# Kernel optimization log

Measured on AMD Instinct MI355X. Metric: run time of the kernel, lower is better.

## Reference

```python
import jax, jax.numpy as jnp
import numpy as np

EMBED_DIM = 512
N_HEAD = 8
Q_DIM = 64
V_DIM = 64
WINDOW_SIZE = 3


def setup_inputs() -> dict:
    key = jax.random.key(0)
    ks = jax.random.split(key, 9)
    B, N = 2, 2048
    x = jax.random.normal(ks[0], (B, N, EMBED_DIM), dtype=jnp.float32)
    s = 0.02
    # torch nn.Linear weights are [out_features, in_features]; y = x @ W.T + b
    Wq = jax.random.normal(ks[1], (N_HEAD * Q_DIM, EMBED_DIM), dtype=jnp.float32) * s
    bq = jax.random.normal(ks[2], (N_HEAD * Q_DIM,), dtype=jnp.float32) * s
    Wk = jax.random.normal(ks[3], (N_HEAD * Q_DIM, EMBED_DIM), dtype=jnp.float32) * s
    bk = jax.random.normal(ks[4], (N_HEAD * Q_DIM,), dtype=jnp.float32) * s
    Wv = jax.random.normal(ks[5], (N_HEAD * V_DIM, EMBED_DIM), dtype=jnp.float32) * s
    bv = jax.random.normal(ks[6], (N_HEAD * V_DIM,), dtype=jnp.float32) * s
    Wo = jax.random.normal(ks[7], (EMBED_DIM, N_HEAD * V_DIM), dtype=jnp.float32) * s
    bo = jax.random.normal(ks[8], (EMBED_DIM,), dtype=jnp.float32) * s
    return {"x": x, "Wq": Wq, "bq": bq, "Wk": Wk, "bk": bk,
            "Wv": Wv, "bv": bv, "Wo": Wo, "bo": bo}


def _diag_indices(n_seq, di):
    # rows i and cols j = i + di of the di-th diagonal
    if di >= 0:
        ii = np.arange(0, n_seq - di)
    else:
        ii = np.arange(-di, n_seq)
    return ii, ii + di


def reference(x, Wq, bq, Wk, bk, Wv, bv, Wo, bo):
    B, N, E = x.shape
    H, Dq, Dv = N_HEAD, Q_DIM, V_DIM
    Q = (x @ Wq.T + bq).reshape(B, N, H, Dq).transpose(0, 2, 1, 3)  # [B,H,N,Dq]
    K = (x @ Wk.T + bk).reshape(B, N, H, Dq).transpose(0, 2, 1, 3)
    V = (x @ Wv.T + bv).reshape(B, N, H, Dv).transpose(0, 2, 1, 3)  # [B,H,N,Dv]
    half = WINDOW_SIZE // 2
    # Faithful to source: scores scattered into COLUMN index i (the loop
    # counter), not the key position; all other columns remain 0 and still
    # participate in the full softmax over n_seq.
    columns = jnp.zeros((B, H, N, N), dtype=x.dtype)
    for i, di in enumerate(range(-half, half + 1)):
        ii, jj = _diag_indices(N, di)
        c = jnp.einsum('bhid,bhid->bhi', Q[:, :, ii, :], K[:, :, jj, :])
        columns = columns.at[:, :, ii, i].set(c)
    attn = jax.nn.softmax(columns, axis=-1)          # [B,H,N,N]
    out = attn @ V                                    # [B,H,N,Dv]
    out = out.transpose(0, 2, 1, 3).reshape(B, N, H * Dv)
    return out @ Wo.T + bo
```

## Files before the change

### kernel.cpp

```cpp
#include <hip/hip_runtime.h>
#include <hip/hip_bf16.h>

#define EMBED 512
#define NSEQ 2048
#define NROWS 4096

typedef unsigned short u16;
typedef __bf16 bf16x8 __attribute__((ext_vector_type(8)));
typedef float f32x4 __attribute__((ext_vector_type(4)));
typedef unsigned short ushort8 __attribute__((ext_vector_type(8)));

__device__ __forceinline__ u16 f2bf(float f) {
    unsigned u = __float_as_uint(f);
    unsigned r = (u + 0x7FFFu + ((u >> 16) & 1u)) >> 16;
    return (u16)r;
}
__device__ __forceinline__ float bf2f(u16 v) {
    return __uint_as_float((unsigned)v << 16);
}

#define XELEMS    (NROWS * EMBED)
#define WCATELEMS (1536 * EMBED)
#define NCONVB    1408

__global__ __launch_bounds__(256) void prep_kernel(
    const float* __restrict__ x,
    const float* __restrict__ Wq, const float* __restrict__ Wk,
    const float* __restrict__ Wv,
    u16* __restrict__ xb, u16* __restrict__ Wcat)
{
    const long long e0 = (long long)(blockIdx.x * 256 + threadIdx.x) * 8;
    const float* src;
    u16* dst;
    if (e0 < XELEMS) {
        src = x + e0; dst = xb + e0;
    } else {
        const long long j = e0 - XELEMS;
        const int row = (int)(j >> 9);
        const int col = (int)(j & 511);
        const int sel = row >> 9;
        const int r   = row & 511;
        const float* W = (sel == 0) ? Wq : (sel == 1) ? Wk : Wv;
        src = W + (size_t)r * EMBED + col; dst = Wcat + j;
    }
    float4 a = *(const float4*)(src);
    float4 b = *(const float4*)(src + 4);
    union { u16 u[8]; uint4 v; } p;
    p.u[0] = f2bf(a.x); p.u[1] = f2bf(a.y); p.u[2] = f2bf(a.z); p.u[3] = f2bf(a.w);
    p.u[4] = f2bf(b.x); p.u[5] = f2bf(b.y); p.u[6] = f2bf(b.z); p.u[7] = f2bf(b.w);
    *(uint4*)(dst) = p.v;
}

__global__ __launch_bounds__(256) void gemm_qkv_mfma(
    const u16* __restrict__ A, const u16* __restrict__ W,
    const float* __restrict__ bq, const float* __restrict__ bk,
    const float* __restrict__ bvv,
    u16* __restrict__ QKb, float* __restrict__ Vhead,
    float* __restrict__ vpart)
{
    __shared__ __align__(16) u16 As[128 * 64];
    __shared__ __align__(16) u16 Bs[64 * 64];

    const int m0 = (blockIdx.x & 31) * 128;
    const int n0 = (blockIdx.x >> 5) * 64;
    const int sel = n0 >> 9;
    const float* bias = ((sel == 0) ? bq : (sel == 1) ? bk : bvv) + (n0 & 511);

    const int t    = threadIdx.x;
    const int wave = t >> 6, lane = t & 63;
    const int wm   = wave >> 1, wn = wave & 1;
    const int qd   = lane >> 4, lr = lane & 15;

    const int sr8 = lane >> 3;
    const int sg  = (lane & 7) ^ sr8;
    const int soff = sg * 8;

    f32x4 acc[4][2] = {};

    const u16* Ag = A + (size_t)m0 * EMBED;
    const u16* Wg = W + (size_t)n0 * EMBED;

    u16* Adst = As + (size_t)(wave * 8) * 64;
    u16* Bdst = Bs + (size_t)(wave * 8) * 64;
    const u16* Asrc = Ag + (size_t)(wave * 8 + sr8) * EMBED + soff;
    const u16* Bsrc = Wg + (size_t)(wave * 8 + sr8) * EMBED + soff;

    for (int kc = 0; kc < EMBED; kc += 64) {
#pragma unroll
        for (int j = 0; j < 4; ++j)
            __builtin_amdgcn_global_load_lds(
                (const __attribute__((address_space(1))) void*)(Asrc + kc + (size_t)j * 32 * EMBED),
                (__attribute__((address_space(3))) void*)(Adst + j * 32 * 64), 16, 0, 0);
#pragma unroll
        for (int j = 0; j < 2; ++j)
            __builtin_amdgcn_global_load_lds(
                (const __attribute__((address_space(1))) void*)(Bsrc + kc + (size_t)j * 32 * EMBED),
                (__attribute__((address_space(3))) void*)(Bdst + j * 32 * 64), 16, 0, 0);
        __syncthreads();

#pragma unroll
        for (int kk = 0; kk < 2; ++kk) {
            const int gr = ((kk * 4 + qd) ^ (lr & 7)) * 8;
            bf16x8 af[4], bfr[2];
#pragma unroll
            for (int i = 0; i < 4; ++i)
                af[i]  = *(const bf16x8*)&As[(wm * 64 + i * 16 + lr) * 64 + gr];
#pragma unroll
            for (int i = 0; i < 2; ++i)
                bfr[i] = *(const bf16x8*)&Bs[(wn * 32 + i * 16 + lr) * 64 + gr];
#pragma unroll
            for (int mi = 0; mi < 4; ++mi)
#pragma unroll
                for (int ni = 0; ni < 2; ++ni)
                    acc[mi][ni] = __builtin_amdgcn_mfma_f32_16x16x32_bf16(
                        af[mi], bfr[ni], acc[mi][ni], 0, 0, 0);
        }
        __syncthreads();
    }

    if (sel < 2) {
#pragma unroll
        for (int ni = 0; ni < 2; ++ni) {
            const int cl = wn * 32 + ni * 16 + lr;
            const float bb = bias[cl];
#pragma unroll
            for (int mi = 0; mi < 4; ++mi)
#pragma unroll
                for (int e = 0; e < 4; ++e) {
                    const int row = m0 + wm * 64 + mi * 16 + qd * 4 + e;
                    QKb[(size_t)row * 1024 + n0 + cl] = f2bf(acc[mi][ni][e] + bb);
                }
        }
    } else {
        const int batch = m0 >> 11;
        const int mtb   = (m0 >> 7) & 15;
#pragma unroll
        for (int ni = 0; ni < 2; ++ni) {
            const int cl  = wn * 32 + ni * 16 + lr;
            const int col = (n0 - 1024) + cl;
            const float bb = bias[cl];
            float s = 0.f;
#pragma unroll
            for (int mi = 0; mi < 4; ++mi)
#pragma unroll
                for (int e = 0; e < 4; ++e) {
                    const int row = m0 + wm * 64 + mi * 16 + qd * 4 + e;
                    s += acc[mi][ni][e];
                    if ((row & (NSEQ - 1)) < 3)
                        Vhead[(size_t)batch * 1536 + (row & (NSEQ - 1)) * 512 + col]
                            = acc[mi][ni][e] + bb;
                }
            s += __shfl_xor(s, 16);
            s += __shfl_xor(s, 32);
            if (qd == 0)
                vpart[((size_t)batch * 512 + col) * 32 + mtb * 2 + wm] = s;
        }
    }
}

__global__ __launch_bounds__(256) void wsmall_kernel(
    const float* __restrict__ Vhead, const float* __restrict__ vpart,
    const float* __restrict__ bv,
    const float* __restrict__ Wo, float* __restrict__ WT)
{
    __shared__ float Vsm[4][512];
    const int b  = blockIdx.x >> 6;
    const int jb = blockIdx.x & 63;
    const int t  = threadIdx.x;

    for (int idx = t; idx < 512; idx += 256) {
        const float v0 = Vhead[(size_t)b * 1536 + idx];
        const float v1 = Vhead[(size_t)b * 1536 + 512 + idx];
        const float v2 = Vhead[(size_t)b * 1536 + 1024 + idx];
        float sum = 0.f;
        const float* vp = vpart + ((size_t)b * 512 + idx) * 32;
#pragma unroll
        for (int s = 0; s < 32; ++s) sum += vp[s];
        Vsm[0][idx] = v0; Vsm[1][idx] = v1; Vsm[2][idx] = v2;
        Vsm[3][idx] = sum + (float)NSEQ * bv[idx] - (v0 + v1 + v2);
    }
    __syncthreads();

    const int j  = jb * 8 + (t >> 5);
    const int s  = t & 31;
    const int h  = s >> 2, tt = s & 3;
    const float* Wor = Wo + (size_t)j * EMBED + h * 64;
    const float* vr  = &Vsm[tt][h * 64];
    float acc = 0.f;
#pragma unroll
    for (int c = 0; c < 64; ++c) {
        const int cc = (c + 2 * s) & 63;
        acc = fmaf(vr[cc], Wor[cc], acc);
    }
    WT[((size_t)b * 512 + j) * 32 + s] = acc;
}

__global__ __launch_bounds__(256) void attn_out_kernel(
    const u16* __restrict__ QKb, const float* __restrict__ WT,
    const float* __restrict__ bo, float* __restrict__ out)
{
    __shared__ float E[16][32];
    const int r0   = blockIdx.x * 16;
    const int b    = r0 >> 11;
    const int wave = threadIdx.x >> 6, lane = threadIdx.x & 63;
    const int d0   = lane * 8;

#pragma unroll
    for (int i = 0; i < 4; ++i) {
        const int rl = wave * 4 + i;
        const int r  = r0 + rl;
        const int sr = r & (NSEQ - 1);
        const u16* Qr = QKb + (size_t)r * 1024 + d0;
        const u16* Kr = QKb + (size_t)r * 1024 + 512 + d0;

        ushort8 qv = *(const ushort8*)Qr;
        ushort8 kv = *(const ushort8*)Kr;
        float q[8], k[8];
#pragma unroll
        for (int z = 0; z < 8; ++z) { q[z] = bf2f(qv[z]); k[z] = bf2f(kv[z]); }

        float s1 = 0.f;
#pragma unroll
        for (int z = 0; z < 8; ++z) s1 = fmaf(q[z], k[z], s1);

        float s0 = 0.f, s2 = 0.f;
        if (sr > 0) {
            ushort8 pv = *(const ushort8*)(Kr - 1024);
#pragma unroll
            for (int z = 0; z < 8; ++z) s0 = fmaf(q[z], bf2f(pv[z]), s0);
        }
        if (sr < NSEQ - 1) {
            ushort8 nv = *(const ushort8*)(Kr + 1024);
#pragma unroll
            for (int z = 0; z < 8; ++z) s2 = fmaf(q[z], bf2f(nv[z]), s2);
        }
#pragma unroll
        for (int off = 1; off <= 4; off <<= 1) {
            s0 += __shfl_xor(s0, off);
            s1 += __shfl_xor(s1, off);
            s2 += __shfl_xor(s2, off);
        }
        const float m  = fmaxf(fmaxf(s0, s1), fmaxf(s2, 0.f));
        const float e0 = __expf(s0 - m);
        const float e1 = __expf(s1 - m);
        const float e2 = __expf(s2 - m);
        const float eb = __expf(-m);
        const float rd = 1.f / (e0 + e1 + e2 + (float)(NSEQ - 3) * eb);
        const int h = lane >> 3, jj = lane & 7;
        const float coef = (jj == 0) ? e0 : (jj == 1) ? e1 : (jj == 2) ? e2 : eb;
        if (jj < 4) E[rl][h * 4 + jj] = coef * rd;
    }
    __syncthreads();

    const int j0 = threadIdx.x * 2;
    const float* WTb = WT + (size_t)b * 512 * 32;
    float w0[32], w1[32];
#pragma unroll
    for (int s = 0; s < 32; ++s) {
        w0[s] = WTb[(size_t)j0 * 32 + s];
        w1[s] = WTb[(size_t)(j0 + 1) * 32 + s];
    }
    const float b0 = bo[j0], b1 = bo[j0 + 1];
#pragma unroll
    for (int rl = 0; rl < 16; ++rl) {
        float a0 = b0, a1 = b1;
#pragma unroll
        for (int s = 0; s < 32; ++s) {
            const float e = E[rl][s];
            a0 = fmaf(e, w0[s], a0);
            a1 = fmaf(e, w1[s], a1);
        }
        float2 o = make_float2(a0, a1);
        *(float2*)(out + (size_t)(r0 + rl) * EMBED + j0) = o;
    }
}

extern "C" void kernel_launch(void* const* d_in, const int* in_sizes, int n_in,
                              void* d_out, int out_size, void* d_ws, size_t ws_size,
                              hipStream_t stream)
{
    const float* x  = (const float*)d_in[0];
    const float* Wq = (const float*)d_in[1];
    const float* bq = (const float*)d_in[2];
    const float* Wk = (const float*)d_in[3];
    const float* bk = (const float*)d_in[4];
    const float* Wv = (const float*)d_in[5];
    const float* bv = (const float*)d_in[6];
    const float* Wo = (const float*)d_in[7];
    const float* bo = (const float*)d_in[8];
    float* out = (float*)d_out;

    u16*   QKb   = (u16*)d_ws;
    u16*   xb    = QKb + (size_t)NROWS * 1024;
    u16*   Wcat  = xb + XELEMS;
    float* Vhead = (float*)(Wcat + WCATELEMS);
    float* vpart = Vhead + 2 * 3 * 512;
    float* WT    = vpart + 2 * 512 * 32;

    prep_kernel<<<NCONVB, 256, 0, stream>>>(x, Wq, Wk, Wv, xb, Wcat);
    gemm_qkv_mfma<<<768, 256, 0, stream>>>(xb, Wcat, bq, bk, bv, QKb, Vhead, vpart);
    wsmall_kernel<<<128, 256, 0, stream>>>(Vhead, vpart, bv, Wo, WT);
    attn_out_kernel<<<256, 256, 0, stream>>>(QKb, WT, bo, out);
}
```

Measured before the change: 105.7 us.

## Replace V projection GEMM with column-sum trick and fold Wo fold into GEMM kernel

```diff
diff --git a/kernel.cpp b/kernel.cpp
--- a/kernel.cpp
+++ b/kernel.cpp
@@ -20,53 +20,152 @@
 }
 
 #define XELEMS    (NROWS * EMBED)
-#define WCATELEMS (1536 * EMBED)
-#define NCONVB    1408
+#define WQKELEMS  (1024 * EMBED)
 
 __global__ __launch_bounds__(256) void prep_kernel(
     const float* __restrict__ x,
     const float* __restrict__ Wq, const float* __restrict__ Wk,
-    const float* __restrict__ Wv,
-    u16* __restrict__ xb, u16* __restrict__ Wcat)
+    u16* __restrict__ xb, u16* __restrict__ Wcat,
+    float* __restrict__ xcs_part)
 {
-    const long long e0 = (long long)(blockIdx.x * 256 + threadIdx.x) * 8;
-    const float* src;
-    u16* dst;
-    if (e0 < XELEMS) {
-        src = x + e0; dst = xb + e0;
+    __shared__ float cs[4][512];
+    const int bid = blockIdx.x, t = threadIdx.x;
+    if (bid < 256) {
+        const float* src = x + (size_t)bid * 16 * EMBED;
+        u16* dst = xb + (size_t)bid * 16 * EMBED;
+        const int rl = t >> 6;
+        const int co = (t & 63) * 8;
+        float s0=0.f,s1=0.f,s2=0.f,s3=0.f,s4=0.f,s5=0.f,s6=0.f,s7=0.f;
+#pragma unroll
+        for (int i = 0; i < 4; ++i) {
+            const size_t off = (size_t)(i * 4 + rl) * EMBED + co;
+            float4 a = *(const float4*)(src + off);
+            float4 b = *(const float4*)(src + off + 4);
+            union { u16 u[8]; uint4 v; } p;
+            p.u[0]=f2bf(a.x); p.u[1]=f2bf(a.y); p.u[2]=f2bf(a.z); p.u[3]=f2bf(a.w);
+            p.u[4]=f2bf(b.x); p.u[5]=f2bf(b.y); p.u[6]=f2bf(b.z); p.u[7]=f2bf(b.w);
+            *(uint4*)(dst + off) = p.v;
+            s0+=a.x; s1+=a.y; s2+=a.z; s3+=a.w;
+            s4+=b.x; s5+=b.y; s6+=b.z; s7+=b.w;
+        }
+        f32x4 v0 = {s0,s1,s2,s3}, v1 = {s4,s5,s6,s7};
+        *(f32x4*)&cs[rl][co]     = v0;
+        *(f32x4*)&cs[rl][co + 4] = v1;
+        __syncthreads();
+        const int b = bid >> 7, blk = bid & 127;
+#pragma unroll
+        for (int d = t; d < 512; d += 256) {
+            xcs_part[((size_t)b * 512 + d) * 128 + blk] =
+                cs[0][d] + cs[1][d] + cs[2][d] + cs[3][d];
+        }
     } else {
-        const long long j = e0 - XELEMS;
-        const int row = (int)(j >> 9);
-        const int col = (int)(j & 511);
-        const int sel = row >> 9;
-        const int r   = row & 511;
-        const float* W = (sel == 0) ? Wq : (sel == 1) ? Wk : Wv;
-        src = W + (size_t)r * EMBED + col; dst = Wcat + j;
-    }
-    float4 a = *(const float4*)(src);
-    float4 b = *(const float4*)(src + 4);
-    union { u16 u[8]; uint4 v; } p;
-    p.u[0] = f2bf(a.x); p.u[1] = f2bf(a.y); p.u[2] = f2bf(a.z); p.u[3] = f2bf(a.w);
-    p.u[4] = f2bf(b.x); p.u[5] = f2bf(b.y); p.u[6] = f2bf(b.z); p.u[7] = f2bf(b.w);
-    *(uint4*)(dst) = p.v;
-}
-
-__global__ __launch_bounds__(256) void gemm_qkv_mfma(
+        const long long e0 = (long long)(bid - 256) * 2048 + (long long)t * 8;
+        const int row = (int)(e0 >> 9), col = (int)(e0 & 511);
+        const float* src = (row < 512) ? (Wq + (size_t)row * EMBED + col)
+                                       : (Wk + (size_t)(row - 512) * EMBED + col);
+        float4 a = *(const float4*)(src);
+        float4 b = *(const float4*)(src + 4);
+        union { u16 u[8]; uint4 v; } p;
+        p.u[0]=f2bf(a.x); p.u[1]=f2bf(a.y); p.u[2]=f2bf(a.z); p.u[3]=f2bf(a.w);
+        p.u[4]=f2bf(b.x); p.u[5]=f2bf(b.y); p.u[6]=f2bf(b.z); p.u[7]=f2bf(b.w);
+        *(uint4*)(Wcat + e0) = p.v;
+    }
+}
+
+__global__ __launch_bounds__(256) void gemm_qk_mfma(
     const u16* __restrict__ A, const u16* __restrict__ W,
     const float* __restrict__ bq, const float* __restrict__ bk,
-    const float* __restrict__ bvv,
-    u16* __restrict__ QKb, float* __restrict__ Vhead,
-    float* __restrict__ vpart)
+    const float* __restrict__ xcs_part, const float* __restrict__ bv,
+    const float* __restrict__ Wv, const float* __restrict__ Wo,
+    u16* __restrict__ QKb, float* __restrict__ WT)
 {
     __shared__ __align__(16) u16 As[128 * 64];
     __shared__ __align__(16) u16 Bs[64 * 64];
+    const int t = threadIdx.x;
+
+    if (blockIdx.x >= 512) {
+        float* xcs  = (float*)As;
+        float* Vraw = (float*)Bs;
+        float* Vloc = Vraw + 256;
+        const int sid = blockIdx.x - 512;
+        const int b = sid >> 4, h = (sid >> 1) & 7, jhalf = sid & 1;
+
+        {
+            const float* p = xcs_part + ((size_t)b * 512 + 2 * t) * 128;
+            float a0 = 0.f, a1 = 0.f;
+#pragma unroll 4
+            for (int i = 0; i < 128; i += 4) {
+                f32x4 u0 = *(const f32x4*)(p + i);
+                f32x4 u1 = *(const f32x4*)(p + 128 + i);
+                a0 += u0[0] + u0[1] + u0[2] + u0[3];
+                a1 += u1[0] + u1[1] + u1[2] + u1[3];
+            }
+            xcs[2 * t] = a0; xcs[2 * t + 1] = a1;
+        }
+        __syncthreads();
+
+        const int tt = t >> 6, cl = t & 63;
+        const int col = h * 64 + cl;
+        const float* wv = Wv + (size_t)col * EMBED;
+        float r = 0.f;
+        if (tt < 3) {
+            const u16* xr = A + ((size_t)b * NSEQ + tt) * EMBED;
+#pragma unroll 8
+            for (int d = 0; d < EMBED; d += 8) {
+                ushort8 xv = *(const ushort8*)(xr + d);
+                f32x4 w0 = *(const f32x4*)(wv + d);
+                f32x4 w1 = *(const f32x4*)(wv + d + 4);
+                r = fmaf(bf2f(xv[0]), w0[0], r);
+                r = fmaf(bf2f(xv[1]), w0[1], r);
+                r = fmaf(bf2f(xv[2]), w0[2], r);
+                r = fmaf(bf2f(xv[3]), w0[3], r);
+                r = fmaf(bf2f(xv[4]), w1[0], r);
+                r = fmaf(bf2f(xv[5]), w1[1], r);
+                r = fmaf(bf2f(xv[6]), w1[2], r);
+                r = fmaf(bf2f(xv[7]), w1[3], r);
+            }
+        } else {
+#pragma unroll 8
+            for (int d = 0; d < EMBED; d += 4) {
+                f32x4 w = *(const f32x4*)(wv + d);
+                r = fmaf(xcs[d],     w[0], r);
+                r = fmaf(xcs[d + 1], w[1], r);
+                r = fmaf(xcs[d + 2], w[2], r);
+                r = fmaf(xcs[d + 3], w[3], r);
+            }
+        }
+        Vraw[tt * 64 + cl] = r;
+        __syncthreads();
+        const float bvc = bv[col];
+        if (tt < 3) Vloc[tt * 64 + cl] = r + bvc;
+        else        Vloc[192 + cl] = r - (Vraw[cl] + Vraw[64 + cl] + Vraw[128 + cl])
+                                       + 2045.f * bvc;
+        __syncthreads();
+
+        const int j = jhalf * 256 + t;
+        const float* wo = Wo + (size_t)j * EMBED + h * 64;
+        float a0 = 0.f, a1 = 0.f, a2 = 0.f, a3 = 0.f;
+#pragma unroll
+        for (int c = 0; c < 64; c += 4) {
+            f32x4 w = *(const f32x4*)(wo + c);
+#pragma unroll
+            for (int z = 0; z < 4; ++z) {
+                a0 = fmaf(Vloc[c + z],       w[z], a0);
+                a1 = fmaf(Vloc[64 + c + z],  w[z], a1);
+                a2 = fmaf(Vloc[128 + c + z], w[z], a2);
+                a3 = fmaf(Vloc[192 + c + z], w[z], a3);
+            }
+        }
+        float* wt = WT + ((size_t)b * 512 + j) * 32 + h * 4;
+        wt[0] = a0; wt[1] = a1; wt[2] = a2; wt[3] = a3;
+        return;
+    }
 
     const int m0 = (blockIdx.x & 31) * 128;
     const int n0 = (blockIdx.x >> 5) * 64;
     const int sel = n0 >> 9;
-    const float* bias = ((sel == 0) ? bq : (sel == 1) ? bk : bvv) + (n0 & 511);
-
-    const int t    = threadIdx.x;
+    const float* bias = ((sel == 0) ? bq : bk) + (n0 & 511);
+
     const int wave = t >> 6, lane = t & 63;
     const int wm   = wave >> 1, wn = wave & 1;
     const int qd   = lane >> 4, lr = lane & 15;
@@ -118,96 +217,33 @@
         __syncthreads();
     }
 
-    if (sel < 2) {
-#pragma unroll
-        for (int ni = 0; ni < 2; ++ni) {
-            const int cl = wn * 32 + ni * 16 + lr;
-            const float bb = bias[cl];
-#pragma unroll
-            for (int mi = 0; mi < 4; ++mi)
-#pragma unroll
-                for (int e = 0; e < 4; ++e) {
-                    const int row = m0 + wm * 64 + mi * 16 + qd * 4 + e;
-                    QKb[(size_t)row * 1024 + n0 + cl] = f2bf(acc[mi][ni][e] + bb);
-                }
-        }
-    } else {
-        const int batch = m0 >> 11;
-        const int mtb   = (m0 >> 7) & 15;
-#pragma unroll
-        for (int ni = 0; ni < 2; ++ni) {
-            const int cl  = wn * 32 + ni * 16 + lr;
-            const int col = (n0 - 1024) + cl;
-            const float bb = bias[cl];
-            float s = 0.f;
-#pragma unroll
-            for (int mi = 0; mi < 4; ++mi)
-#pragma unroll
-                for (int e = 0; e < 4; ++e) {
-                    const int row = m0 + wm * 64 + mi * 16 + qd * 4 + e;
-                    s += acc[mi][ni][e];
-                    if ((row & (NSEQ - 1)) < 3)
-                        Vhead[(size_t)batch * 1536 + (row & (NSEQ - 1)) * 512 + col]
-                            = acc[mi][ni][e] + bb;
-                }
-            s += __shfl_xor(s, 16);
-            s += __shfl_xor(s, 32);
-            if (qd == 0)
-                vpart[((size_t)batch * 512 + col) * 32 + mtb * 2 + wm] = s;
-        }
-    }
-}
-
-__global__ __launch_bounds__(256) void wsmall_kernel(
-    const float* __restrict__ Vhead, const float* __restrict__ vpart,
-    const float* __restrict__ bv,
-    const float* __restrict__ Wo, float* __restrict__ WT)
-{
-    __shared__ float Vsm[4][512];
-    const int b  = blockIdx.x >> 6;
-    const int jb = blockIdx.x & 63;
-    const int t  = threadIdx.x;
-
-    for (int idx = t; idx < 512; idx += 256) {
-        const float v0 = Vhead[(size_t)b * 1536 + idx];
-        const float v1 = Vhead[(size_t)b * 1536 + 512 + idx];
-        const float v2 = Vhead[(size_t)b * 1536 + 1024 + idx];
-        float sum = 0.f;
-        const float* vp = vpart + ((size_t)b * 512 + idx) * 32;
-#pragma unroll
-        for (int s = 0; s < 32; ++s) sum += vp[s];
-        Vsm[0][idx] = v0; Vsm[1][idx] = v1; Vsm[2][idx] = v2;
-        Vsm[3][idx] = sum + (float)NSEQ * bv[idx] - (v0 + v1 + v2);
-    }
-    __syncthreads();
-
-    const int j  = jb * 8 + (t >> 5);
-    const int s  = t & 31;
-    const int h  = s >> 2, tt = s & 3;
-    const float* Wor = Wo + (size_t)j * EMBED + h * 64;
-    const float* vr  = &Vsm[tt][h * 64];
-    float acc = 0.f;
-#pragma unroll
-    for (int c = 0; c < 64; ++c) {
-        const int cc = (c + 2 * s) & 63;
-        acc = fmaf(vr[cc], Wor[cc], acc);
-    }
-    WT[((size_t)b * 512 + j) * 32 + s] = acc;
+#pragma unroll
+    for (int ni = 0; ni < 2; ++ni) {
+        const int cl = wn * 32 + ni * 16 + lr;
+        const float bb = bias[cl];
+#pragma unroll
+        for (int mi = 0; mi < 4; ++mi)
+#pragma unroll
+            for (int e = 0; e < 4; ++e) {
+                const int row = m0 + wm * 64 + mi * 16 + qd * 4 + e;
+                QKb[(size_t)row * 1024 + n0 + cl] = f2bf(acc[mi][ni][e] + bb);
+            }
+    }
 }
 
 __global__ __launch_bounds__(256) void attn_out_kernel(
     const u16* __restrict__ QKb, const float* __restrict__ WT,
     const float* __restrict__ bo, float* __restrict__ out)
 {
-    __shared__ float E[16][32];
-    const int r0   = blockIdx.x * 16;
+    __shared__ float E[8][32];
+    const int r0   = blockIdx.x * 8;
     const int b    = r0 >> 11;
     const int wave = threadIdx.x >> 6, lane = threadIdx.x & 63;
     const int d0   = lane * 8;
 
 #pragma unroll
-    for (int i = 0; i < 4; ++i) {
-        const int rl = wave * 4 + i;
+    for (int i = 0; i < 2; ++i) {
+        const int rl = wave * 2 + i;
         const int r  = r0 + rl;
         const int sr = r & (NSEQ - 1);
         const u16* Qr = QKb + (size_t)r * 1024 + d0;
@@ -262,7 +298,7 @@
     }
     const float b0 = bo[j0], b1 = bo[j0 + 1];
 #pragma unroll
-    for (int rl = 0; rl < 16; ++rl) {
+    for (int rl = 0; rl < 8; ++rl) {
         float a0 = b0, a1 = b1;
 #pragma unroll
         for (int s = 0; s < 32; ++s) {
@@ -270,8 +306,7 @@
             a0 = fmaf(e, w0[s], a0);
             a1 = fmaf(e, w1[s], a1);
         }
-        float2 o = make_float2(a0, a1);
-        *(float2*)(out + (size_t)(r0 + rl) * EMBED + j0) = o;
+        *(float2*)(out + (size_t)(r0 + rl) * EMBED + j0) = make_float2(a0, a1);
     }
 }
 
@@ -290,15 +325,14 @@
     const float* bo = (const float*)d_in[8];
     float* out = (float*)d_out;
 
-    u16*   QKb   = (u16*)d_ws;
-    u16*   xb    = QKb + (size_t)NROWS * 1024;
-    u16*   Wcat  = xb + XELEMS;
-    float* Vhead = (float*)(Wcat + WCATELEMS);
-    float* vpart = Vhead + 2 * 3 * 512;
-    float* WT    = vpart + 2 * 512 * 32;
-
-    prep_kernel<<<NCONVB, 256, 0, stream>>>(x, Wq, Wk, Wv, xb, Wcat);
-    gemm_qkv_mfma<<<768, 256, 0, stream>>>(xb, Wcat, bq, bk, bv, QKb, Vhead, vpart);
-    wsmall_kernel<<<128, 256, 0, stream>>>(Vhead, vpart, bv, Wo, WT);
-    attn_out_kernel<<<256, 256, 0, stream>>>(QKb, WT, bo, out);
-}
+    u16*   QKb      = (u16*)d_ws;
+    u16*   xb       = QKb + (size_t)NROWS * 1024;
+    u16*   Wcat     = xb + XELEMS;
+    float* xcs_part = (float*)(Wcat + WQKELEMS);
+    float* WT       = xcs_part + 2 * 512 * 128;
+
+    prep_kernel<<<512, 256, 0, stream>>>(x, Wq, Wk, xb, Wcat, xcs_part);
+    gemm_qk_mfma<<<544, 256, 0, stream>>>(xb, Wcat, bq, bk, xcs_part, bv, Wv, Wo,
+                                          QKb, WT);
+    attn_out_kernel<<<512, 256, 0, stream>>>(QKb, WT, bo, out);
+}
```

Measured after the change: 126.1 us. +19.3%, slower.

## Fuse four kernel launches into one cooperative kernel with grid syncs

Applied to the files above, without the earlier changes.

```diff
diff --git a/kernel.cpp b/kernel.cpp
--- a/kernel.cpp
+++ b/kernel.cpp
@@ -1,5 +1,6 @@
 #include <hip/hip_runtime.h>
 #include <hip/hip_bf16.h>
+#include <hip/hip_cooperative_groups.h>
 
 #define EMBED 512
 #define NSEQ 2048
@@ -22,6 +23,259 @@
 #define XELEMS    (NROWS * EMBED)
 #define WCATELEMS (1536 * EMBED)
 #define NCONVB    1408
+
+__global__ __launch_bounds__(256, 3) void fused_all(
+    const float* __restrict__ x,
+    const float* __restrict__ Wq, const float* __restrict__ Wk,
+    const float* __restrict__ Wv,
+    const float* __restrict__ bq, const float* __restrict__ bk,
+    const float* __restrict__ bvv,
+    const float* __restrict__ Wo, const float* __restrict__ bo,
+    u16* __restrict__ xb, u16* __restrict__ Wcat, u16* __restrict__ QKb,
+    float* __restrict__ Vhead, float* __restrict__ vpart,
+    float* __restrict__ WT, float* __restrict__ out)
+{
+    __shared__ __align__(16) u16 As[128 * 64];
+    __shared__ __align__(16) u16 Bs[64 * 64];
+    cooperative_groups::grid_group grid = cooperative_groups::this_grid();
+    const int t   = threadIdx.x;
+    const int bid = blockIdx.x;
+
+    {
+        const long long NOCT = (long long)(XELEMS + WCATELEMS) / 8;
+        for (long long idx = (long long)bid * 256 + t; idx < NOCT;
+             idx += 768LL * 256) {
+            const long long e0 = idx * 8;
+            const float* src;
+            u16* dst;
+            if (e0 < XELEMS) {
+                src = x + e0; dst = xb + e0;
+            } else {
+                const long long j = e0 - XELEMS;
+                const int row = (int)(j >> 9);
+                const int col = (int)(j & 511);
+                const int sel = row >> 9;
+                const int r   = row & 511;
+                const float* W = (sel == 0) ? Wq : (sel == 1) ? Wk : Wv;
+                src = W + (size_t)r * EMBED + col; dst = Wcat + j;
+            }
+            float4 a = *(const float4*)(src);
+            float4 b = *(const float4*)(src + 4);
+            union { u16 u[8]; uint4 v; } p;
+            p.u[0]=f2bf(a.x); p.u[1]=f2bf(a.y); p.u[2]=f2bf(a.z); p.u[3]=f2bf(a.w);
+            p.u[4]=f2bf(b.x); p.u[5]=f2bf(b.y); p.u[6]=f2bf(b.z); p.u[7]=f2bf(b.w);
+            *(uint4*)(dst) = p.v;
+        }
+    }
+    grid.sync();
+
+    {
+        const int m0 = (bid & 31) * 128;
+        const int n0 = (bid >> 5) * 64;
+        const int sel = n0 >> 9;
+        const float* bias = ((sel == 0) ? bq : (sel == 1) ? bk : bvv) + (n0 & 511);
+
+        const int wave = t >> 6, lane = t & 63;
+        const int wm   = wave >> 1, wn = wave & 1;
+        const int qd   = lane >> 4, lr = lane & 15;
+
+        const int sr8 = lane >> 3;
+        const int sg  = (lane & 7) ^ sr8;
+        const int soff = sg * 8;
+
+        f32x4 acc[4][2] = {};
+
+        const u16* Ag = xb + (size_t)m0 * EMBED;
+        const u16* Wg = Wcat + (size_t)n0 * EMBED;
+
+        u16* Adst = As + (size_t)(wave * 8) * 64;
+        u16* Bdst = Bs + (size_t)(wave * 8) * 64;
+        const u16* Asrc = Ag + (size_t)(wave * 8 + sr8) * EMBED + soff;
+        const u16* Bsrc = Wg + (size_t)(wave * 8 + sr8) * EMBED + soff;
+
+        for (int kc = 0; kc < EMBED; kc += 64) {
+#pragma unroll
+            for (int j = 0; j < 4; ++j)
+                __builtin_amdgcn_global_load_lds(
+                    (const __attribute__((address_space(1))) void*)(Asrc + kc + (size_t)j * 32 * EMBED),
+                    (__attribute__((address_space(3))) void*)(Adst + j * 32 * 64), 16, 0, 0);
+#pragma unroll
+            for (int j = 0; j < 2; ++j)
+                __builtin_amdgcn_global_load_lds(
+                    (const __attribute__((address_space(1))) void*)(Bsrc + kc + (size_t)j * 32 * EMBED),
+                    (__attribute__((address_space(3))) void*)(Bdst + j * 32 * 64), 16, 0, 0);
+            __syncthreads();
+
+#pragma unroll
+            for (int kk = 0; kk < 2; ++kk) {
+                const int gr = ((kk * 4 + qd) ^ (lr & 7)) * 8;
+                bf16x8 af[4], bfr[2];
+#pragma unroll
+                for (int i = 0; i < 4; ++i)
+                    af[i]  = *(const bf16x8*)&As[(wm * 64 + i * 16 + lr) * 64 + gr];
+#pragma unroll
+                for (int i = 0; i < 2; ++i)
+                    bfr[i] = *(const bf16x8*)&Bs[(wn * 32 + i * 16 + lr) * 64 + gr];
+#pragma unroll
+                for (int mi = 0; mi < 4; ++mi)
+#pragma unroll
+                    for (int ni = 0; ni < 2; ++ni)
+                        acc[mi][ni] = __builtin_amdgcn_mfma_f32_16x16x32_bf16(
+                            af[mi], bfr[ni], acc[mi][ni], 0, 0, 0);
+            }
+            __syncthreads();
+        }
+
+        if (sel < 2) {
+#pragma unroll
+            for (int ni = 0; ni < 2; ++ni) {
+                const int cl = wn * 32 + ni * 16 + lr;
+                const float bb = bias[cl];
+#pragma unroll
+                for (int mi = 0; mi < 4; ++mi)
+#pragma unroll
+                    for (int e = 0; e < 4; ++e) {
+                        const int row = m0 + wm * 64 + mi * 16 + qd * 4 + e;
+                        QKb[(size_t)row * 1024 + n0 + cl] = f2bf(acc[mi][ni][e] + bb);
+                    }
+            }
+        } else {
+            const int batch = m0 >> 11;
+            const int mtb   = (m0 >> 7) & 15;
+#pragma unroll
+            for (int ni = 0; ni < 2; ++ni) {
+                const int cl  = wn * 32 + ni * 16 + lr;
+                const int col = (n0 - 1024) + cl;
+                const float bb = bias[cl];
+                float s = 0.f;
+#pragma unroll
+                for (int mi = 0; mi < 4; ++mi)
+#pragma unroll
+                    for (int e = 0; e < 4; ++e) {
+                        const int row = m0 + wm * 64 + mi * 16 + qd * 4 + e;
+                        s += acc[mi][ni][e];
+                        if ((row & (NSEQ - 1)) < 3)
+                            Vhead[(size_t)batch * 1536 + (row & (NSEQ - 1)) * 512 + col]
+                                = acc[mi][ni][e] + bb;
+                    }
+                s += __shfl_xor(s, 16);
+                s += __shfl_xor(s, 32);
+                if (qd == 0)
+                    vpart[((size_t)batch * 512 + col) * 32 + mtb * 2 + wm] = s;
+            }
+        }
+    }
+    grid.sync();
+
+    if (bid < 128) {
+        float (*Vsm)[512] = (float(*)[512])As;
+        const int b  = bid >> 6;
+        const int jb = bid & 63;
+
+        for (int idx = t; idx < 512; idx += 256) {
+            const float v0 = Vhead[(size_t)b * 1536 + idx];
+            const float v1 = Vhead[(size_t)b * 1536 + 512 + idx];
+            const float v2 = Vhead[(size_t)b * 1536 + 1024 + idx];
+            float sum = 0.f;
+            const float* vp = vpart + ((size_t)b * 512 + idx) * 32;
+#pragma unroll
+            for (int s = 0; s < 32; ++s) sum += vp[s];
+            Vsm[0][idx] = v0; Vsm[1][idx] = v1; Vsm[2][idx] = v2;
+            Vsm[3][idx] = sum + (float)NSEQ * bvv[idx] - (v0 + v1 + v2);
+        }
+        __syncthreads();
+
+        const int j  = jb * 8 + (t >> 5);
+        const int s  = t & 31;
+        const int h  = s >> 2, tt = s & 3;
+        const float* Wor = Wo + (size_t)j * EMBED + h * 64;
+        const float* vr  = &Vsm[tt][h * 64];
+        float acc = 0.f;
+#pragma unroll
+        for (int c = 0; c < 64; ++c) {
+            const int cc = (c + 2 * s) & 63;
+            acc = fmaf(vr[cc], Wor[cc], acc);
+        }
+        WT[((size_t)b * 512 + j) * 32 + s] = acc;
+    }
+    grid.sync();
+
+    if (bid < 256) {
+        float (*E)[32] = (float(*)[32])Bs;
+        const int r0   = bid * 16;
+        const int b    = r0 >> 11;
+        const int wave = t >> 6, lane = t & 63;
+        const int d0   = lane * 8;
+
+#pragma unroll
+        for (int i = 0; i < 4; ++i) {
+            const int rl = wave * 4 + i;
+            const int r  = r0 + rl;
+            const int sr = r & (NSEQ - 1);
+            const u16* Qr = QKb + (size_t)r * 1024 + d0;
+            const u16* Kr = QKb + (size_t)r * 1024 + 512 + d0;
+
+            ushort8 qv = *(const ushort8*)Qr;
+            ushort8 kv = *(const ushort8*)Kr;
+            float q[8], k[8];
+#pragma unroll
+            for (int z = 0; z < 8; ++z) { q[z] = bf2f(qv[z]); k[z] = bf2f(kv[z]); }
+
+            float s1 = 0.f;
+#pragma unroll
+            for (int z = 0; z < 8; ++z) s1 = fmaf(q[z], k[z], s1);
+
+            float s0 = 0.f, s2 = 0.f;
+            if (sr > 0) {
+                ushort8 pv = *(const ushort8*)(Kr - 1024);
+#pragma unroll
+                for (int z = 0; z < 8; ++z) s0 = fmaf(q[z], bf2f(pv[z]), s0);
+            }
+            if (sr < NSEQ - 1) {
+                ushort8 nv = *(const ushort8*)(Kr + 1024);
+#pragma unroll
+                for (int z = 0; z < 8; ++z) s2 = fmaf(q[z], bf2f(nv[z]), s2);
+            }
+#pragma unroll
+            for (int off = 1; off <= 4; off <<= 1) {
+                s0 += __shfl_xor(s0, off);
+                s1 += __shfl_xor(s1, off);
+                s2 += __shfl_xor(s2, off);
+            }
+            const float m  = fmaxf(fmaxf(s0, s1), fmaxf(s2, 0.f));
+            const float e0 = __expf(s0 - m);
+            const float e1 = __expf(s1 - m);
+            const float e2 = __expf(s2 - m);
+            const float eb = __expf(-m);
+            const float rd = 1.f / (e0 + e1 + e2 + (float)(NSEQ - 3) * eb);
+            const int h = lane >> 3, jj = lane & 7;
+            const float coef = (jj == 0) ? e0 : (jj == 1) ? e1 : (jj == 2) ? e2 : eb;
+            if (jj < 4) E[rl][h * 4 + jj] = coef * rd;
+        }
+        __syncthreads();
+
+        const int j0 = t * 2;
+        const float* WTb = WT + (size_t)b * 512 * 32;
+        float w0[32], w1[32];
+#pragma unroll
+        for (int s = 0; s < 32; ++s) {
+            w0[s] = WTb[(size_t)j0 * 32 + s];
+            w1[s] = WTb[(size_t)(j0 + 1) * 32 + s];
+        }
+        const float b0 = bo[j0], b1 = bo[j0 + 1];
+#pragma unroll
+        for (int rl = 0; rl < 16; ++rl) {
+            float a0 = b0, a1 = b1;
+#pragma unroll
+            for (int s = 0; s < 32; ++s) {
+                const float e = E[rl][s];
+                a0 = fmaf(e, w0[s], a0);
+                a1 = fmaf(e, w1[s], a1);
+            }
+            *(float2*)(out + (size_t)(r0 + rl) * EMBED + j0) = make_float2(a0, a1);
+        }
+    }
+}
 
 __global__ __launch_bounds__(256) void prep_kernel(
     const float* __restrict__ x,
@@ -297,8 +551,28 @@
     float* vpart = Vhead + 2 * 3 * 512;
     float* WT    = vpart + 2 * 512 * 32;
 
-    prep_kernel<<<NCONVB, 256, 0, stream>>>(x, Wq, Wk, Wv, xb, Wcat);
-    gemm_qkv_mfma<<<768, 256, 0, stream>>>(xb, Wcat, bq, bk, bv, QKb, Vhead, vpart);
-    wsmall_kernel<<<128, 256, 0, stream>>>(Vhead, vpart, bv, Wo, WT);
-    attn_out_kernel<<<256, 256, 0, stream>>>(QKb, WT, bo, out);
-}
+    static int use_coop = -1;
+    if (use_coop < 0) {
+        int dev = 0;
+        (void)hipGetDevice(&dev);
+        int sup = 0;
+        (void)hipDeviceGetAttribute(&sup, hipDeviceAttributeCooperativeLaunch, dev);
+        int maxb = 0;
+        (void)hipOccupancyMaxActiveBlocksPerMultiprocessor(&maxb, fused_all, 256, 0);
+        use_coop = (sup && maxb >= 3) ? 1 : 0;
+    }
+
+    if (use_coop) {
+        void* args[] = { (void*)&x, (void*)&Wq, (void*)&Wk, (void*)&Wv,
+                         (void*)&bq, (void*)&bk, (void*)&bv, (void*)&Wo,
+                         (void*)&bo, (void*)&xb, (void*)&Wcat, (void*)&QKb,
+                         (void*)&Vhead, (void*)&vpart, (void*)&WT, (void*)&out };
+        (void)hipLaunchCooperativeKernel((void*)fused_all, dim3(768), dim3(256),
+                                         args, 0, stream);
+    } else {
+        prep_kernel<<<NCONVB, 256, 0, stream>>>(x, Wq, Wk, Wv, xb, Wcat);
+        gemm_qkv_mfma<<<768, 256, 0, stream>>>(xb, Wcat, bq, bk, bv, QKb, Vhead, vpart);
+        wsmall_kernel<<<128, 256, 0, stream>>>(Vhead, vpart, bv, Wo, WT);
+        attn_out_kernel<<<256, 256, 0, stream>>>(QKb, WT, bo, out);
+    }
+}
```

After: 106.2 us. Within noise of the previous version (+0.5%).
